# Optimization experiments

Measured on AMD Instinct MI355X. Metric: run time of the kernel, lower is better.

## Reference

```python
import jax, jax.numpy as jnp
import numpy as np

NUM_HEADS = 16


def setup_inputs() -> dict:
    key = jax.random.key(0)
    k1, k2, k3, k4, k5 = jax.random.split(key, 5)
    B, N, C = 4, 1370, 1024
    s = 0.02
    return {
        "tokens": jax.random.normal(k1, (B, N, C), jnp.float32),
        "qkv_w": jax.random.normal(k2, (3 * C, C), jnp.float32) * s,
        "qkv_b": jax.random.normal(k3, (3 * C,), jnp.float32) * s,
        "proj_w": jax.random.normal(k4, (C, C), jnp.float32) * s,
        "proj_b": jax.random.normal(k5, (C,), jnp.float32) * s,
    }


def reference(tokens, qkv_w, qkv_b, proj_w, proj_b):
    B, N, C = tokens.shape
    H = NUM_HEADS
    c = C // H
    scale = c ** (-0.5)
    # qkv projection: [B,N,3C] -> [3,B,H,N,c]
    qkv = tokens @ qkv_w.T + qkv_b
    qkv = qkv.reshape(B, N, 3, H, c).transpose(2, 0, 3, 1, 4)
    q, k, v = qkv[0], qkv[1], qkv[2]
    q = q * scale
    attn = jnp.einsum("bhqc,bhkc->bhqk", q, k)  # [B,H,N,N]
    w = jax.nn.softmax(attn, axis=-1)
    out = jnp.einsum("bhqk,bhkc->bhqc", w, v)  # [B,H,N,c]
    out = out.transpose(0, 2, 1, 3).reshape(B, N, C)
    return out @ proj_w.T + proj_b
```

## Files before the change

### kernel.cpp

```cpp
#include <hip/hip_runtime.h>
#include <hip/hip_bf16.h>

typedef short s16x8 __attribute__((ext_vector_type(8)));
typedef float f32x4 __attribute__((ext_vector_type(4)));
typedef float f32x16 __attribute__((ext_vector_type(16)));
typedef unsigned short u16;
typedef unsigned int   u32;
typedef u16 u16x4 __attribute__((ext_vector_type(4)));

#define SEQ  1370
#define CH   1024
#define NH   16
#define HD   64
#define BN   5480
#define MPAD 5504
#define NPAD 1408
#define NQT  43
#define NKT64 22

#define QSCALE 0.18033688f


__device__ __forceinline__ u16 f2bf(float f){
  union { float f; unsigned u; } v; v.f = f;
  unsigned u = v.u;
  return (u16)((u + 0x7FFFu + ((u >> 16) & 1u)) >> 16);
}

__device__ __forceinline__ u32 cvt_pk_bf16(float lo, float hi){
  u32 r;
  asm("v_cvt_pk_bf16_f32 %0, %1, %2" : "=v"(r) : "v"(lo), "v"(hi));
  return r;
}

#define GLOAD16(gp, lp) __builtin_amdgcn_global_load_lds( \
    (const __attribute__((address_space(1))) void*)(gp), \
    (__attribute__((address_space(3))) void*)(lp), 16, 0, 0)

#define CAST_O0 (MPAD*CH)
#define CAST_O1 (CAST_O0 + 3*CH*CH)
#define CAST_TOT (CAST_O1 + CH*CH)

__global__ __launch_bounds__(256) void k_cast_all(
    const float* __restrict__ tokens, const float* __restrict__ qkv_w,
    const float* __restrict__ proj_w, u16* __restrict__ Xbf,
    u16* __restrict__ Wqkv, u16* __restrict__ Wproj)
{
  int i8 = (blockIdx.x * 256 + threadIdx.x) * 8;
  if(i8 >= CAST_TOT) return;
  const float* src; u16* dst; int off;
  if(i8 < CAST_O0){
    int row = i8 >> 10;
    s16x8 o = {0,0,0,0,0,0,0,0};
    if(row < BN){
      f32x4 a = *reinterpret_cast<const f32x4*>(tokens + i8);
      f32x4 b = *reinterpret_cast<const f32x4*>(tokens + i8 + 4);
#pragma unroll
      for(int j=0;j<4;j++){ o[j] = (short)f2bf(a[j]); o[4+j] = (short)f2bf(b[j]); }
    }
    *reinterpret_cast<s16x8*>(Xbf + i8) = o;
    return;
  } else if(i8 < CAST_O1){
    src = qkv_w; dst = Wqkv; off = i8 - CAST_O0;
  } else {
    src = proj_w; dst = Wproj; off = i8 - CAST_O1;
  }
  f32x4 a = *reinterpret_cast<const f32x4*>(src + off);
  f32x4 b = *reinterpret_cast<const f32x4*>(src + off + 4);
  s16x8 o;
#pragma unroll
  for(int j=0;j<4;j++){ o[j] = (short)f2bf(a[j]); o[4+j] = (short)f2bf(b[j]); }
  *reinterpret_cast<s16x8*>(dst + off) = o;
}

template<int MODE, int NT>
__global__ __launch_bounds__(256,4) void k_gemm128(
    const u16* __restrict__ A, const u16* __restrict__ Bw, const float* __restrict__ bias,
    u16* __restrict__ q, u16* __restrict__ kk_, u16* __restrict__ vv, float* __restrict__ out)
{
  constexpr int NF = NT/32;
  __shared__ u16 As[128*64];
  __shared__ u16 Bs[NT*64];
  const int t = threadIdx.x;
  const int lane = t & 63;
  const int w = t >> 6;
  const int wm = w >> 1, wn = w & 1;
  const int g = lane >> 4, lr = lane & 15;

  const int bid = blockIdx.x;
  const int xcd = bid & 7, idx = bid >> 3;
  const int xr = xcd & 3, yr = xcd >> 2;
  constexpr int YLOC = (MODE == 0) ? 12 : 8;
  const int x = xr*11 + idx % 11;
  const int y = yr*YLOC + idx / 11;
  if(x >= MPAD/128) return;
  const int m0 = x*128, n0 = y*NT;

  const int swc = ((t & 7) ^ ((t >> 3) & 7)) * 8;
  const u16* ga0 = A  + (size_t)(m0 + (t >> 3)) * 1024 + swc;
  const u16* gb0 = Bw + (size_t)(n0 + (t >> 3)) * 1024 + swc;

  f32x4 z = {0.f,0.f,0.f,0.f};
  f32x4 acc[4][NF];
#pragma unroll
  for(int mf=0;mf<4;mf++)
#pragma unroll
    for(int nf=0;nf<NF;nf++) acc[mf][nf] = z;

  for(int k0 = 0; k0 < 1024; k0 += 64){
#pragma unroll
    for(int j=0;j<4;j++)
      GLOAD16(ga0 + k0 + j*32*1024, As + j*2048 + w*512);
#pragma unroll
    for(int j=0;j<NF;j++)
      GLOAD16(gb0 + k0 + j*32*1024, Bs + j*2048 + w*512);
    __syncthreads();
#pragma unroll
    for(int kk=0; kk<2; kk++){
      s16x8 af[4], bf[NF];
#pragma unroll
      for(int mf = 0; mf < 4; mf++)
        af[mf] = *reinterpret_cast<const s16x8*>(&As[(wm*64 + mf*16 + lr)*64 + ((kk*4+g) ^ (lr&7))*8]);
#pragma unroll
      for(int nf = 0; nf < NF; nf++)
        bf[nf] = *reinterpret_cast<const s16x8*>(&Bs[(wn*16*NF + nf*16 + lr)*64 + ((kk*4+g) ^ (lr&7))*8]);
#pragma unroll
      for(int mf = 0; mf < 4; mf++)
#pragma unroll
        for(int nf = 0; nf < NF; nf++)
          acc[mf][nf] = __builtin_amdgcn_mfma_f32_16x16x32_bf16(af[mf], bf[nf], acc[mf][nf], 0,0,0);
    }
    __syncthreads();
  }

#pragma unroll
  for(int mf = 0; mf < 4; mf++){
#pragma unroll
    for(int nf = 0; nf < NF; nf++){
      int colc = n0 + wn*16*NF + nf*16 + lr;
      float bb = bias[colc];
      if constexpr (MODE == 0){
        int tt = colc >> 10, h = (colc >> 6) & 15, cc = colc & 63;
        const int rowb = m0 + wm*64 + mf*16 + g*4;
        if(tt == 2){
          int b = rowb / SEQ;
          int nb = rowb - b*SEQ;
          if(rowb + 3 < BN && nb + 4 <= SEQ && (nb & 3) == 0){
            int bh = b*NH + h;
            int ktv = nb >> 6, kh = (nb >> 4) & 3, hiv = (nb >> 3) & 1;
            int e0 = nb & 7;
            int dtv = cc >> 5, colr = cc & 31;
            u16x4 ov;
#pragma unroll
            for(int r=0;r<4;r++) ov[r] = f2bf(acc[mf][nf][r] + bb);
            *reinterpret_cast<u16x4*>(vv +
              (size_t)((((bh*22 + ktv)*4 + kh)*2 + dtv)*2 + hiv)*256 + colr*8 + e0) = ov;
          } else {
#pragma unroll
            for(int r = 0; r < 4; r++){
              int row = rowb + r;
              if(row >= BN) continue;
              int b2 = row / SEQ, n = row - b2*SEQ;
              int bh = b2*NH + h;
              int ktv = n >> 6, kh = (n >> 4) & 3, hiv = (n >> 3) & 1, e = n & 7;
              int dtv = cc >> 5, colr = cc & 31;
              vv[(size_t)((((bh*22 + ktv)*4 + kh)*2 + dtv)*2 + hiv)*256 + colr*8 + e]
                = f2bf(acc[mf][nf][r] + bb);
            }
          }
        } else {
#pragma unroll
          for(int r = 0; r < 4; r++){
            int row = rowb + r;
            if(row >= BN) continue;
            int b = row / SEQ, n = row - b*SEQ;
            int bh = b*NH + h;
            int gg = n >> 5, colr = n & 31;
            int dtv = cc >> 4, hiq = (cc >> 3) & 1, e = cc & 7;
            size_t fidx = (size_t)(((bh*44 + gg)*4 + dtv)*2 + hiq)*256 + colr*8 + e;
            float v = acc[mf][nf][r] + bb;
            if(tt == 0) q  [fidx] = f2bf(v * QSCALE);
            else        kk_[fidx] = f2bf(v);
          }
        }
      } else {
#pragma unroll
        for(int r = 0; r < 4; r++){
          int row = m0 + wm*64 + mf*16 + g*4 + r;
          if(row >= BN) continue;
          out[(size_t)row * CH + colc] = acc[mf][nf][r] + bb;
        }
      }
    }
  }
}

__global__ __launch_bounds__(256,3) void k_attn9(
    const u16* __restrict__ Qf, const u16* __restrict__ Kf,
    const u16* __restrict__ Vf, u16* __restrict__ O)
{
  __shared__ u16 Kl[2][4096];
  __shared__ u16 Vl[2][4096];
  const int bid = blockIdx.x;
  const int swz = (bid & 7)*88 + (bid >> 3);
  const int bh = swz / 11;
  const int qg = swz - bh*11;
  const int w = threadIdx.x >> 6;
  int qt = qg*4 + w;
  const bool wr = (qt < NQT);
  if(!wr) qt = NQT - 1;
  const int lane = threadIdx.x & 63;
  const int col = lane & 31;
  const int hi  = lane >> 5;
  const int n0  = qt * 32;
  const int lofs = hi*256 + col*8;

  s16x8 qf[4];
  {
    const u16* qfb = Qf + (size_t)(bh*44 + qt)*2048 + lofs;
#pragma unroll
    for(int dt=0; dt<4; dt++)
      qf[dt] = *reinterpret_cast<const s16x8*>(qfb + dt*512);
  }
  const u16* kfb = Kf + (size_t)bh*44*2048;
  const u16* vfb = Vf + (size_t)bh*22*4096;

#define STAGE_T(KT, CB) { \
  const u16* gk_ = kfb + (size_t)(KT)*4096 + w*1024 + lane*8; \
  const u16* gv_ = vfb + (size_t)(KT)*4096 + w*1024 + lane*8; \
  GLOAD16(gk_,       &Kl[CB][w*1024]); \
  GLOAD16(gk_ + 512, &Kl[CB][w*1024 + 512]); \
  GLOAD16(gv_,       &Vl[CB][w*1024]); \
  GLOAD16(gv_ + 512, &Vl[CB][w*1024 + 512]); }

  f32x16 accO[2];
  f32x16 accL;
#pragma unroll
  for(int i=0;i<16;i++){ accO[0][i]=0.f; accO[1][i]=0.f; accL[i]=0.f; }
  const s16x8 onesf = {(short)0x3F80,(short)0x3F80,(short)0x3F80,(short)0x3F80,
                       (short)0x3F80,(short)0x3F80,(short)0x3F80,(short)0x3F80};

  STAGE_T(0, 0);
  asm volatile("s_waitcnt vmcnt(0)" ::: "memory");
  __builtin_amdgcn_s_barrier();

  for(int kt = 0; kt < NKT64; kt++){
    const int kj0 = kt * 64;
    const int cur = kt & 1;
    if(kt + 1 < NKT64) STAGE_T(kt + 1, cur^1);
    f32x16 St[2];
#pragma unroll
    for(int s=0;s<2;s++){
#pragma unroll
      for(int i=0;i<16;i++) St[s][i]=0.f;
#pragma unroll
      for(int dt=0;dt<4;dt++){
        s16x8 kf = *reinterpret_cast<const s16x8*>(&Kl[cur][s*2048 + dt*512 + lofs]);
        St[s] = __builtin_amdgcn_mfma_f32_32x32x16_bf16(kf, qf[dt], St[s], 0,0,0);
      }
    }
    float p[32];
    if(kj0 + 64 <= SEQ){
#pragma unroll
      for(int i=0;i<32;i++) p[i] = exp2f(St[i>>4][i&15]);
    } else {
#pragma unroll
      for(int s=0;s<2;s++)
#pragma unroll
        for(int r=0;r<16;r++){
          int k = kj0 + s*32 + (r&3) + 8*(r>>2) + 4*hi;
          p[s*16+r] = (k < SEQ) ? exp2f(St[s][r]) : 0.f;
        }
    }
    union PF { u32 w[4]; s16x8 v; } pf[4];
#pragma unroll
    for(int s=0;s<2;s++){
#pragma unroll
      for(int hh=0; hh<2; hh++){
        const int b0 = s*16 + hh*8;
        u32 w0 = cvt_pk_bf16(p[b0+0], p[b0+1]);
        u32 w1 = cvt_pk_bf16(p[b0+2], p[b0+3]);
        u32 w2 = cvt_pk_bf16(p[b0+4], p[b0+5]);
        u32 w3 = cvt_pk_bf16(p[b0+6], p[b0+7]);
        auto r02 = __builtin_amdgcn_permlane32_swap(w0, w2, false, false);
        auto r13 = __builtin_amdgcn_permlane32_swap(w1, w3, false, false);
        pf[s*2+hh].w[0] = r02[0];
        pf[s*2+hh].w[1] = r13[0];
        pf[s*2+hh].w[2] = r02[1];
        pf[s*2+hh].w[3] = r13[1];
      }
    }
#pragma unroll
    for(int kh=0; kh<4; kh++){
#pragma unroll
      for(int dt=0; dt<2; dt++){
        s16x8 vf = *reinterpret_cast<const s16x8*>(&Vl[cur][(kh*2+dt)*512 + lofs]);
        accO[dt] = __builtin_amdgcn_mfma_f32_32x32x16_bf16(vf, pf[kh].v, accO[dt], 0,0,0);
      }
      accL = __builtin_amdgcn_mfma_f32_32x32x16_bf16(onesf, pf[kh].v, accL, 0,0,0);
    }
    asm volatile("s_waitcnt vmcnt(0)" ::: "memory");
    __builtin_amdgcn_s_barrier();
  }

  const int n = n0 + col;
  if(wr && n < SEQ){
    float inv = 1.0f / accL[0];
    const int b = bh >> 4, h = bh & 15;
    u16* orow = O + ((size_t)(b*SEQ + n))*CH + h*HD;
#pragma unroll
    for(int dt=0; dt<2; dt++)
#pragma unroll
      for(int qd=0; qd<4; qd++){
        u16x4 ov;
#pragma unroll
        for(int j=0;j<4;j++) ov[j] = f2bf(accO[dt][qd*4+j]*inv);
        *reinterpret_cast<u16x4*>(orow + dt*32 + qd*8 + hi*4) = ov;
      }
  }
}

extern "C" void kernel_launch(void* const* d_in, const int* in_sizes, int n_in,
                              void* d_out, int out_size, void* d_ws, size_t ws_size,
                              hipStream_t stream)
{
  const float* tokens = (const float*)d_in[0];
  const float* qkv_w  = (const float*)d_in[1];
  const float* qkv_b  = (const float*)d_in[2];
  const float* proj_w = (const float*)d_in[3];
  const float* proj_b = (const float*)d_in[4];
  float* out = (float*)d_out;

  char* ws = (char*)d_ws;
  u16* Xbf   = (u16*)(ws);
  u16* Wqkv  = (u16*)(ws + 11272192);
  u16* Wproj = (u16*)(ws + 17563648);
  u16* Qfb   = (u16*)(ws + 19660800);
  u16* Kfb   = (u16*)(ws + 31195136);
  u16* Vfb   = (u16*)(ws + 42729472);
  u16* AttO  = (u16*)(ws + 65798144);

  k_cast_all<<<dim3(CAST_TOT/2048), 256, 0, stream>>>(tokens, qkv_w, proj_w, Xbf, Wqkv, Wproj);

  k_gemm128<0,128><<<dim3(1056), 256, 0, stream>>>(Xbf, Wqkv, qkv_b, Qfb, Kfb, Vfb, nullptr);
  k_attn9<<<dim3(704), 256, 0, stream>>>(Qfb, Kfb, Vfb, AttO);
  k_gemm128<1,64><<<dim3(704), 256, 0, stream>>>(AttO, Wproj, proj_b, nullptr, nullptr, nullptr, out);
}
```

Before: 150.4 us.

## Split attention keys across two blocks and merge partial results

Splits the key dimension of attention into two halves handled by separate blocks (split-K), doubling the grid from 704 to 1408 blocks and raising the occupancy hint to 4. Each half writes unnormalised partial outputs in bf16 plus row sums, and a new merge kernel adds them and normalises. This targets poor CU fill, since 704 blocks is a small count for the GPU, at the cost of an extra kernel launch, extra global traffic, and an extra bf16 rounding of the partial outputs. It relies on the softmax having no max subtraction, so partial sums can simply be added.

Result: slower. 155.5 us (+3.4%).

```diff
diff --git a/kernel.cpp b/kernel.cpp
--- a/kernel.cpp
+++ b/kernel.cpp
@@ -20,11 +20,15 @@
 
 #define QSCALE 0.18033688f
 
-
 __device__ __forceinline__ u16 f2bf(float f){
   union { float f; unsigned u; } v; v.f = f;
   unsigned u = v.u;
   return (u16)((u + 0x7FFFu + ((u >> 16) & 1u)) >> 16);
+}
+
+__device__ __forceinline__ float bf2f(u16 b){
+  union { unsigned u; float f; } v; v.u = ((u32)b) << 16;
+  return v.f;
 }
 
 __device__ __forceinline__ u32 cvt_pk_bf16(float lo, float hi){
@@ -195,13 +199,16 @@
   }
 }
 
-__global__ __launch_bounds__(256,3) void k_attn9(
+__global__ __launch_bounds__(256,4) void k_attn_sk2(
     const u16* __restrict__ Qf, const u16* __restrict__ Kf,
-    const u16* __restrict__ Vf, u16* __restrict__ O)
+    const u16* __restrict__ Vf, u16* __restrict__ NpA, u16* __restrict__ NpB,
+    float* __restrict__ LpA, float* __restrict__ LpB)
 {
   __shared__ u16 Kl[2][4096];
   __shared__ u16 Vl[2][4096];
-  const int bid = blockIdx.x;
+  const int bid2 = blockIdx.x;
+  const int half = bid2 & 1;
+  const int bid = bid2 >> 1;
   const int swz = (bid & 7)*88 + (bid >> 3);
   const int bh = swz / 11;
   const int qg = swz - bh*11;
@@ -240,14 +247,15 @@
   const s16x8 onesf = {(short)0x3F80,(short)0x3F80,(short)0x3F80,(short)0x3F80,
                        (short)0x3F80,(short)0x3F80,(short)0x3F80,(short)0x3F80};
 
-  STAGE_T(0, 0);
+  const int kt0 = half * 11, ktE = kt0 + 11;
+  STAGE_T(kt0, kt0 & 1);
   asm volatile("s_waitcnt vmcnt(0)" ::: "memory");
   __builtin_amdgcn_s_barrier();
 
-  for(int kt = 0; kt < NKT64; kt++){
+  for(int kt = kt0; kt < ktE; kt++){
     const int kj0 = kt * 64;
     const int cur = kt & 1;
-    if(kt + 1 < NKT64) STAGE_T(kt + 1, cur^1);
+    if(kt + 1 < ktE) STAGE_T(kt + 1, cur^1);
     f32x16 St[2];
 #pragma unroll
     for(int s=0;s<2;s++){
@@ -303,21 +311,48 @@
     __builtin_amdgcn_s_barrier();
   }
 
-  const int n = n0 + col;
-  if(wr && n < SEQ){
-    float inv = 1.0f / accL[0];
-    const int b = bh >> 4, h = bh & 15;
-    u16* orow = O + ((size_t)(b*SEQ + n))*CH + h*HD;
+  if(wr){
+    u16* np = (half ? NpB : NpA) + (size_t)(bh*43 + qt)*2048 + col*64;
+    float* lp = (half ? LpB : LpA);
 #pragma unroll
     for(int dt=0; dt<2; dt++)
 #pragma unroll
       for(int qd=0; qd<4; qd++){
         u16x4 ov;
 #pragma unroll
-        for(int j=0;j<4;j++) ov[j] = f2bf(accO[dt][qd*4+j]*inv);
-        *reinterpret_cast<u16x4*>(orow + dt*32 + qd*8 + hi*4) = ov;
-      }
-  }
+        for(int j=0;j<4;j++) ov[j] = f2bf(accO[dt][qd*4+j]);
+        *reinterpret_cast<u16x4*>(np + dt*32 + qd*8 + hi*4) = ov;
+      }
+    lp[(bh*43 + qt)*32 + col] = accL[0];
+  }
+}
+
+#define MERGE_TOT (64*43*2048)
+
+__global__ __launch_bounds__(256) void k_merge(
+    const u16* __restrict__ NpA, const u16* __restrict__ NpB,
+    const float* __restrict__ LpA, const float* __restrict__ LpB,
+    u16* __restrict__ OM)
+{
+  int idx8 = (blockIdx.x * 256 + threadIdx.x) * 8;
+  if(idx8 >= MERGE_TOT) return;
+  int bh  = idx8 / (43*2048);
+  int rem = idx8 - bh*(43*2048);
+  int qt  = rem >> 11;
+  int rr  = rem & 2047;
+  int row = rr >> 6, d0 = rr & 63;
+  int n = qt*32 + row;
+  if(n >= SEQ) return;
+  int li = (bh*43 + qt)*32 + row;
+  float inv = 1.0f / (LpA[li] + LpB[li]);
+  s16x8 a = *reinterpret_cast<const s16x8*>(NpA + idx8);
+  s16x8 b = *reinterpret_cast<const s16x8*>(NpB + idx8);
+  s16x8 o;
+#pragma unroll
+  for(int j=0;j<8;j++)
+    o[j] = (short)f2bf((bf2f((u16)a[j]) + bf2f((u16)b[j])) * inv);
+  int bb = bh >> 4, h = bh & 15;
+  *reinterpret_cast<s16x8*>(OM + ((size_t)(bb*SEQ + n))*CH + h*HD + d0) = o;
 }
 
 extern "C" void kernel_launch(void* const* d_in, const int* in_sizes, int n_in,
@@ -339,10 +374,16 @@
   u16* Kfb   = (u16*)(ws + 31195136);
   u16* Vfb   = (u16*)(ws + 42729472);
   u16* AttO  = (u16*)(ws + 65798144);
+  u16*   NpA = (u16*)(ws);
+  float* LpA = (float*)(ws + 11272192);
+  float* LpB = (float*)(ws + 11624448);
+  u16*   NpB = AttO;
+  u16*   OM  = Qfb;
 
   k_cast_all<<<dim3(CAST_TOT/2048), 256, 0, stream>>>(tokens, qkv_w, proj_w, Xbf, Wqkv, Wproj);
 
   k_gemm128<0,128><<<dim3(1056), 256, 0, stream>>>(Xbf, Wqkv, qkv_b, Qfb, Kfb, Vfb, nullptr);
-  k_attn9<<<dim3(704), 256, 0, stream>>>(Qfb, Kfb, Vfb, AttO);
-  k_gemm128<1,64><<<dim3(704), 256, 0, stream>>>(AttO, Wproj, proj_b, nullptr, nullptr, nullptr, out);
-}
+  k_attn_sk2<<<dim3(1408), 256, 0, stream>>>(Qfb, Kfb, Vfb, NpA, NpB, LpA, LpB);
+  k_merge<<<dim3(MERGE_TOT/2048), 256, 0, stream>>>(NpA, NpB, LpA, LpB, OM);
+  k_gemm128<1,64><<<dim3(704), 256, 0, stream>>>(OM, Wproj, proj_b, nullptr, nullptr, nullptr, out);
+}
```
